# Performance work log

Hardware: AMD Instinct MI355X
Metric: run time of the kernel (lower is better)

## Reference

```python
import jax, jax.numpy as jnp
import numpy as np
import math

D = 2048
N = 4096


def setup_inputs() -> dict:
    key = jax.random.key(0)
    ks = jax.random.split(key, 7)
    s = 1.0 / math.sqrt(D)
    return {
        "x": jax.random.normal(ks[0], (N, D), dtype=jnp.float32),
        "Wq": jax.random.normal(ks[1], (D, D), dtype=jnp.float32) * s,
        "bq": jnp.zeros((D,), dtype=jnp.float32),
        "Wk": jax.random.normal(ks[2], (D, D), dtype=jnp.float32) * s,
        "bk": jnp.zeros((D,), dtype=jnp.float32),
        "Wv": jax.random.normal(ks[3], (D, D), dtype=jnp.float32) * s,
        "bv": jnp.zeros((D,), dtype=jnp.float32),
    }


def reference(x, Wq, bq, Wk, bk, Wv, bv):
    # nn.Linear: y = x @ W.T + b
    q = x @ Wq.T + bq          # [N, D]
    k = x @ Wk.T + bk          # [N, D]
    v = x @ Wv.T + bv          # [N, D]
    # scores = Q K^T / sqrt(input_dim); NOTE: original has NO softmax.
    scores = (q @ k.T) * (1.0 / math.sqrt(D))  # [N, N]
    # dropout p=0.0 -> identity (eval-equivalent)
    context = scores @ v       # [N, D]
    return context
```

## Files before the change

### kernel.cpp

```cpp
#include <hip/hip_runtime.h>
#include <hip/hip_bf16.h>

typedef __hip_bfloat16 bf16;
typedef __attribute__((ext_vector_type(8))) short short8;
typedef __attribute__((ext_vector_type(4))) float floatx4;

#define BK 64

__device__ __forceinline__ void store_out(bf16* p, float v)  { *p = __float2bfloat16(v); }
__device__ __forceinline__ void store_out(float* p, float v) { *p = v; }

template <int TM, int TN, int WR, int WC, typename OutT>
__device__ __forceinline__ void gemm_bt_tile(
    const bf16* __restrict__ A, const bf16* __restrict__ B,
    const float* __restrict__ bias, OutT* __restrict__ C,
    int Kdim, int N, float alpha, int bm, int bn, int bias_mode)
{
    constexpr int FI = TM / (WR * 16);
    constexpr int FJ = TN / (WC * 16);
    __shared__ __attribute__((aligned(16))) bf16 As[TM * BK];
    __shared__ __attribute__((aligned(16))) bf16 Bs[TN * BK];

    const int tid  = threadIdx.x;
    const int lane = tid & 63;
    const int wave = tid >> 6;
    const int wm   = (wave / WC) * (FI * 16);
    const int wn   = (wave % WC) * (FJ * 16);
    const int lr   = lane & 15;
    const int lkc  = lane >> 4;

    floatx4 acc[FI][FJ] = {};

    const bf16* Ab = A + (size_t)(bm * TM) * Kdim;
    const bf16* Bb = B + (size_t)(bn * TN) * Kdim;

    for (int k0 = 0; k0 < Kdim; k0 += BK) {
        __syncthreads();
#pragma unroll
        for (int p = 0; p < TM * 8 / 256; ++p) {
            const int t   = p * 256 + tid;
            const int row = t >> 3;
            const int cg  = (t & 7) ^ (row & 7);
            __builtin_amdgcn_global_load_lds(
                (const __attribute__((address_space(1))) void*)(Ab + (size_t)row * Kdim + k0 + cg * 8),
                (__attribute__((address_space(3))) void*)(As + t * 8), 16, 0, 0);
        }
#pragma unroll
        for (int p = 0; p < TN * 8 / 256; ++p) {
            const int t   = p * 256 + tid;
            const int row = t >> 3;
            const int cg  = (t & 7) ^ (row & 7);
            __builtin_amdgcn_global_load_lds(
                (const __attribute__((address_space(1))) void*)(Bb + (size_t)row * Kdim + k0 + cg * 8),
                (__attribute__((address_space(3))) void*)(Bs + t * 8), 16, 0, 0);
        }
        __syncthreads();

#pragma unroll
        for (int kk = 0; kk < 2; ++kk) {
            const int sw = (((kk << 2) + lkc) ^ (lr & 7)) << 3;
            short8 af[FI], bfr[FJ];
#pragma unroll
            for (int i = 0; i < FI; ++i)
                af[i]  = *(const short8*)(As + (wm + i * 16 + lr) * BK + sw);
#pragma unroll
            for (int j = 0; j < FJ; ++j)
                bfr[j] = *(const short8*)(Bs + (wn + j * 16 + lr) * BK + sw);
#pragma unroll
            for (int i = 0; i < FI; ++i)
#pragma unroll
                for (int j = 0; j < FJ; ++j)
                    acc[i][j] = __builtin_amdgcn_mfma_f32_16x16x32_bf16(
                        af[i], bfr[j], acc[i][j], 0, 0, 0);
        }
    }

    const int rbase = (lane >> 4) << 2;
#pragma unroll
    for (int i = 0; i < FI; ++i) {
#pragma unroll
        for (int j = 0; j < FJ; ++j) {
            const int n = bn * TN + wn + j * 16 + lr;
#pragma unroll
            for (int r = 0; r < 4; ++r) {
                const int m = bm * TM + wm + i * 16 + rbase + r;
                float v = acc[i][j][r] * alpha;
                if (bias_mode == 1)      v += bias[n];
                else if (bias_mode == 2) v += bias[m];
                store_out(&C[(size_t)m * N + n], v);
            }
        }
    }
}

__global__ __launch_bounds__(256) void cvt_all(
    const float* __restrict__ x, const float* __restrict__ Wq,
    const float* __restrict__ Wk, const float* __restrict__ Wv,
    bf16* __restrict__ dst, int nd4, int dd4)
{
    const int i = blockIdx.x * 256 + threadIdx.x;
    const float* src;
    int off;
    if (i < nd4)                { src = x;  off = i; }
    else if (i < nd4 + dd4)     { src = Wq; off = i - nd4; }
    else if (i < nd4 + 2 * dd4) { src = Wk; off = i - nd4 - dd4; }
    else                        { src = Wv; off = i - nd4 - 2 * dd4; }
    const float4 v = ((const float4*)src)[off];
    bf16 o[4] = {__float2bfloat16(v.x), __float2bfloat16(v.y),
                 __float2bfloat16(v.z), __float2bfloat16(v.w)};
    ((ulong1*)dst)[i] = *(const ulong1*)o;
}

__global__ __launch_bounds__(256) void qkv_gemm(
    const bf16* __restrict__ xb,
    const bf16* __restrict__ Wqb, const float* __restrict__ bq,
    const bf16* __restrict__ Wkb, const float* __restrict__ bk,
    const bf16* __restrict__ Wvb, const float* __restrict__ bv,
    bf16* __restrict__ Q, bf16* __restrict__ Kt, bf16* __restrict__ Vt)
{
    const int z = blockIdx.z;
    if (z == 0)
        gemm_bt_tile<128, 128, 2, 2>(xb, Wqb, bq, Q, 2048, 2048, 1.0f, blockIdx.x, blockIdx.y, 1);
    else if (z == 1)
        gemm_bt_tile<128, 128, 2, 2>(Wkb, xb, bk, Kt, 2048, 4096, 1.0f, blockIdx.y, blockIdx.x, 2);
    else
        gemm_bt_tile<128, 128, 2, 2>(Wvb, xb, bv, Vt, 2048, 4096, 1.0f, blockIdx.y, blockIdx.x, 2);
}

__global__ __launch_bounds__(256) void u_gemm(
    const bf16* __restrict__ Vt, const bf16* __restrict__ Kt, bf16* __restrict__ U)
{
    gemm_bt_tile<128, 64, 2, 2>(Vt, Kt, nullptr, U, 4096, 2048, 1.0f,
                                blockIdx.x, blockIdx.y, 0);
}

__global__ __launch_bounds__(256) void out_gemm(
    const bf16* __restrict__ Q, const bf16* __restrict__ U, float* __restrict__ out)
{
    gemm_bt_tile<128, 128, 2, 2>(Q, U, nullptr, out, 2048, 2048,
                                 0.022097086912079608f, blockIdx.x, blockIdx.y, 0);
}

extern "C" void kernel_launch(void* const* d_in, const int* in_sizes, int n_in,
                              void* d_out, int out_size, void* d_ws, size_t ws_size,
                              hipStream_t stream)
{
    const float* x  = (const float*)d_in[0];
    const float* Wq = (const float*)d_in[1];
    const float* bq = (const float*)d_in[2];
    const float* Wk = (const float*)d_in[3];
    const float* bk = (const float*)d_in[4];
    const float* Wv = (const float*)d_in[5];
    const float* bv = (const float*)d_in[6];
    float* out = (float*)d_out;

    const size_t ND = (size_t)4096 * 2048;
    const size_t DD = (size_t)2048 * 2048;

    bf16* xb  = (bf16*)d_ws;
    bf16* Wqb = xb  + ND;
    bf16* Wkb = Wqb + DD;
    bf16* Wvb = Wkb + DD;
    bf16* Q   = Wvb + DD;
    bf16* Kt  = Q   + ND;
    bf16* Vt  = Kt  + ND;
    bf16* U   = Vt  + ND;

    const int nd4 = (int)(ND / 4), dd4 = (int)(DD / 4);
    cvt_all<<<(nd4 + 3 * dd4) / 256, 256, 0, stream>>>(x, Wq, Wk, Wv, xb, nd4, dd4);

    qkv_gemm<<<dim3(32, 16, 3), 256, 0, stream>>>(xb, Wqb, bq, Wkb, bk, Wvb, bv, Q, Kt, Vt);
    u_gemm<<<dim3(16, 32), 256, 0, stream>>>(Vt, Kt, U);
    out_gemm<<<dim3(32, 16), 256, 0, stream>>>(Q, U, out);
}
```

Before: 335.3 us.

## Reassociate attention chain through Gram matrix x^T x to shrink GEMM sizes

Since there is no softmax, the output is x·(Wq^T·(Wv·(Wk·(x^T x))^T)^T)·scale plus bias terms. The code computes the Gram matrix G = x^T x once, then chains three D×D GEMMs and one N×D output GEMM, handling the biases with a rank-2 correction and matvecs. This replaces the three N×D projections and the N-dimension reductions with fewer total FLOPs. In exchange it adds several small launches (transposes, colsum with atomics, matvecs) and rounds each intermediate D×D product to bf16, which adds precision error.

```diff
diff --git a/kernel.cpp b/kernel.cpp
--- a/kernel.cpp
+++ b/kernel.cpp
@@ -3,9 +3,11 @@
 
 typedef __hip_bfloat16 bf16;
 typedef __attribute__((ext_vector_type(8))) short short8;
+typedef __attribute__((ext_vector_type(4))) short shortx4;
 typedef __attribute__((ext_vector_type(4))) float floatx4;
 
 #define BK 64
+#define RSQRT_D 0.022097086912079608f
 
 __device__ __forceinline__ void store_out(bf16* p, float v)  { *p = __float2bfloat16(v); }
 __device__ __forceinline__ void store_out(float* p, float v) { *p = v; }
@@ -85,8 +87,7 @@
             for (int r = 0; r < 4; ++r) {
                 const int m = bm * TM + wm + i * 16 + rbase + r;
                 float v = acc[i][j][r] * alpha;
-                if (bias_mode == 1)      v += bias[n];
-                else if (bias_mode == 2) v += bias[m];
+                if (bias_mode == 1) v += bias[n];
                 store_out(&C[(size_t)m * N + n], v);
             }
         }
@@ -94,51 +95,120 @@
 }
 
 __global__ __launch_bounds__(256) void cvt_all(
-    const float* __restrict__ x, const float* __restrict__ Wq,
-    const float* __restrict__ Wk, const float* __restrict__ Wv,
-    bf16* __restrict__ dst, int nd4, int dd4)
+    const float* __restrict__ x, const float* __restrict__ Wk,
+    const float* __restrict__ Wv, bf16* __restrict__ dst, int nd4, int dd4)
 {
     const int i = blockIdx.x * 256 + threadIdx.x;
     const float* src;
     int off;
-    if (i < nd4)                { src = x;  off = i; }
-    else if (i < nd4 + dd4)     { src = Wq; off = i - nd4; }
-    else if (i < nd4 + 2 * dd4) { src = Wk; off = i - nd4 - dd4; }
-    else                        { src = Wv; off = i - nd4 - 2 * dd4; }
+    if (i < nd4)            { src = x;  off = i; }
+    else if (i < nd4 + dd4) { src = Wk; off = i - nd4; }
+    else                    { src = Wv; off = i - nd4 - dd4; }
     const float4 v = ((const float4*)src)[off];
     bf16 o[4] = {__float2bfloat16(v.x), __float2bfloat16(v.y),
                  __float2bfloat16(v.z), __float2bfloat16(v.w)};
     ((ulong1*)dst)[i] = *(const ulong1*)o;
 }
 
-__global__ __launch_bounds__(256) void qkv_gemm(
-    const bf16* __restrict__ xb,
-    const bf16* __restrict__ Wqb, const float* __restrict__ bq,
-    const bf16* __restrict__ Wkb, const float* __restrict__ bk,
-    const bf16* __restrict__ Wvb, const float* __restrict__ bv,
-    bf16* __restrict__ Q, bf16* __restrict__ Kt, bf16* __restrict__ Vt)
-{
-    const int z = blockIdx.z;
-    if (z == 0)
-        gemm_bt_tile<128, 128, 2, 2>(xb, Wqb, bq, Q, 2048, 2048, 1.0f, blockIdx.x, blockIdx.y, 1);
-    else if (z == 1)
-        gemm_bt_tile<128, 128, 2, 2>(Wkb, xb, bk, Kt, 2048, 4096, 1.0f, blockIdx.y, blockIdx.x, 2);
-    else
-        gemm_bt_tile<128, 128, 2, 2>(Wvb, xb, bv, Vt, 2048, 4096, 1.0f, blockIdx.y, blockIdx.x, 2);
-}
-
-__global__ __launch_bounds__(256) void u_gemm(
-    const bf16* __restrict__ Vt, const bf16* __restrict__ Kt, bf16* __restrict__ U)
-{
-    gemm_bt_tile<128, 64, 2, 2>(Vt, Kt, nullptr, U, 4096, 2048, 1.0f,
-                                blockIdx.x, blockIdx.y, 0);
-}
-
+__global__ __launch_bounds__(256) void transpose_f32_bf16(
+    const float* __restrict__ src, bf16* __restrict__ dst, int R, int C)
+{
+    __shared__ bf16 Lt[64][72];
+    const int t  = threadIdx.x;
+    const int r0 = t >> 4;
+    const int c0 = (t & 15) * 4;
+    const int gr = blockIdx.y * 64;
+    const int gc = blockIdx.x * 64;
+#pragma unroll
+    for (int i = 0; i < 4; ++i) {
+        const int rl = r0 + i * 16;
+        const float4 v = *(const float4*)(src + (size_t)(gr + rl) * C + gc + c0);
+        Lt[c0 + 0][rl] = __float2bfloat16(v.x);
+        Lt[c0 + 1][rl] = __float2bfloat16(v.y);
+        Lt[c0 + 2][rl] = __float2bfloat16(v.z);
+        Lt[c0 + 3][rl] = __float2bfloat16(v.w);
+    }
+    __syncthreads();
+#pragma unroll
+    for (int i = 0; i < 4; ++i) {
+        const int cl = r0 + i * 16;
+        *(shortx4*)(dst + (size_t)(gc + cl) * R + gr + c0) =
+            *(const shortx4*)&Lt[cl][c0];
+    }
+}
+
+__global__ __launch_bounds__(256) void colsum(
+    const float* __restrict__ x, float* __restrict__ c)
+{
+    const int col = blockIdx.x * 256 + threadIdx.x;
+    const int r0  = blockIdx.y * 256;
+    float s = 0.f;
+    for (int r = 0; r < 256; ++r) s += x[(size_t)(r0 + r) * 2048 + col];
+    atomicAdd(&c[col], s);
+}
+
+__global__ __launch_bounds__(256) void matvec(
+    const bf16* __restrict__ A, const float* __restrict__ v,
+    float* __restrict__ u, float alpha)
+{
+    const int lane = threadIdx.x & 63;
+    const int row  = blockIdx.x * 4 + (threadIdx.x >> 6);
+    float s = 0.f;
+    for (int k = lane; k < 2048; k += 64)
+        s += __bfloat162float(A[(size_t)row * 2048 + k]) * v[k];
+#pragma unroll
+    for (int off = 32; off > 0; off >>= 1) s += __shfl_down(s, off);
+    if (lane == 0) u[row] = s * alpha;
+}
+
+__global__ __launch_bounds__(256) void rank2_update(
+    bf16* __restrict__ P, const float* __restrict__ u2, const float* __restrict__ bk,
+    const float* __restrict__ bv, const float* __restrict__ u1)
+{
+    const int idx4 = (blockIdx.x * 256 + threadIdx.x) * 4;
+    const int i  = idx4 >> 11;
+    const int j0 = idx4 & 2047;
+    bf16 p[4];
+    *(shortx4*)p = *(const shortx4*)(P + idx4);
+#pragma unroll
+    for (int q = 0; q < 4; ++q) {
+        const int j = j0 + q;
+        float v = __bfloat162float(p[q]) + u2[i] * bk[j] + bv[i] * (u1[j] + 4096.f * bk[j]);
+        p[q] = __float2bfloat16(v);
+    }
+    *(shortx4*)(P + idx4) = *(const shortx4*)p;
+}
+
+
+__global__ __launch_bounds__(256) void g_gemm(const bf16* __restrict__ xt, bf16* __restrict__ G)
+{
+    gemm_bt_tile<128, 64, 2, 2>(xt, xt, nullptr, G, 4096, 2048, 1.0f,
+                                blockIdx.x, blockIdx.y, 0);
+}
+__global__ __launch_bounds__(256) void t_gemm(
+    const bf16* __restrict__ Wkb, const bf16* __restrict__ G, bf16* __restrict__ T)
+{
+    gemm_bt_tile<128, 64, 2, 2>(Wkb, G, nullptr, T, 2048, 2048, 1.0f,
+                                blockIdx.x, blockIdx.y, 0);
+}
+__global__ __launch_bounds__(256) void p_gemm(
+    const bf16* __restrict__ Wvb, const bf16* __restrict__ T, bf16* __restrict__ P)
+{
+    gemm_bt_tile<128, 64, 2, 2>(Wvb, T, nullptr, P, 2048, 2048, 1.0f,
+                                blockIdx.x, blockIdx.y, 0);
+}
+__global__ __launch_bounds__(256) void mt_gemm(
+    const bf16* __restrict__ P, const bf16* __restrict__ Wqt, bf16* __restrict__ Mt)
+{
+    gemm_bt_tile<128, 64, 2, 2>(P, Wqt, nullptr, Mt, 2048, 2048, RSQRT_D,
+                                blockIdx.x, blockIdx.y, 0);
+}
 __global__ __launch_bounds__(256) void out_gemm(
-    const bf16* __restrict__ Q, const bf16* __restrict__ U, float* __restrict__ out)
-{
-    gemm_bt_tile<128, 128, 2, 2>(Q, U, nullptr, out, 2048, 2048,
-                                 0.022097086912079608f, blockIdx.x, blockIdx.y, 0);
+    const bf16* __restrict__ xb, const bf16* __restrict__ Mt,
+    const float* __restrict__ r, float* __restrict__ out)
+{
+    gemm_bt_tile<128, 128, 2, 2>(xb, Mt, r, out, 2048, 2048, 1.0f,
+                                 blockIdx.x, blockIdx.y, 1);
 }
 
 extern "C" void kernel_launch(void* const* d_in, const int* in_sizes, int n_in,
@@ -158,18 +228,34 @@
     const size_t DD = (size_t)2048 * 2048;
 
     bf16* xb  = (bf16*)d_ws;
-    bf16* Wqb = xb  + ND;
-    bf16* Wkb = Wqb + DD;
+    bf16* Wkb = xb  + ND;
     bf16* Wvb = Wkb + DD;
-    bf16* Q   = Wvb + DD;
-    bf16* Kt  = Q   + ND;
-    bf16* Vt  = Kt  + ND;
-    bf16* U   = Vt  + ND;
+    bf16* xt  = Wvb + DD;
+    bf16* Wqt = xt  + ND;
+    bf16* G   = Wqt + DD;
+    bf16* T   = G   + DD;
+    bf16* P   = T   + DD;
+    bf16* Mt  = P   + DD;
+    float* c  = (float*)(Mt + DD);
+    float* u1 = c  + 2048;
+    float* u2 = u1 + 2048;
+    float* r  = u2 + 2048;
 
     const int nd4 = (int)(ND / 4), dd4 = (int)(DD / 4);
-    cvt_all<<<(nd4 + 3 * dd4) / 256, 256, 0, stream>>>(x, Wq, Wk, Wv, xb, nd4, dd4);
-
-    qkv_gemm<<<dim3(32, 16, 3), 256, 0, stream>>>(xb, Wqb, bq, Wkb, bk, Wvb, bv, Q, Kt, Vt);
-    u_gemm<<<dim3(16, 32), 256, 0, stream>>>(Vt, Kt, U);
-    out_gemm<<<dim3(32, 16), 256, 0, stream>>>(Q, U, out);
-}
+
+    hipMemsetAsync(c, 0, 2048 * sizeof(float), stream);
+    cvt_all<<<(nd4 + 2 * dd4) / 256, 256, 0, stream>>>(x, Wk, Wv, xb, nd4, dd4);
+    transpose_f32_bf16<<<dim3(32, 64), 256, 0, stream>>>(x,  xt,  4096, 2048);
+    transpose_f32_bf16<<<dim3(32, 32), 256, 0, stream>>>(Wq, Wqt, 2048, 2048);
+    colsum<<<dim3(8, 16), 256, 0, stream>>>(x, c);
+    matvec<<<512, 256, 0, stream>>>(Wkb, c, u1, 1.0f);
+    matvec<<<512, 256, 0, stream>>>(Wvb, c, u2, 1.0f);
+
+    g_gemm <<<dim3(16, 32), 256, 0, stream>>>(xt, G);
+    t_gemm <<<dim3(16, 32), 256, 0, stream>>>(Wkb, G, T);
+    p_gemm <<<dim3(16, 32), 256, 0, stream>>>(Wvb, T, P);
+    rank2_update<<<4096, 256, 0, stream>>>(P, u2, bk, bv, u1);
+    matvec<<<512, 256, 0, stream>>>(P, bq, r, RSQRT_D);
+    mt_gemm<<<dim3(16, 32), 256, 0, stream>>>(P, Wqt, Mt);
+    out_gemm<<<dim3(32, 16), 256, 0, stream>>>(xb, Mt, r, out);
+}
```

Measured after the change: 368.6 us. 10.0% more time.
